# Optimization experiments

Measured on AMD Instinct MI355X. Metric: run time of the kernel, lower is better.

## Reference

```python
import jax, jax.numpy as jnp
import numpy as np

N_NODES = 12288
N_EDGES = 393216
LATENT = 128
EDGE_F = 4


def setup_inputs() -> dict:
    key = jax.random.key(0)
    k1, k2, k3, k4 = jax.random.split(key, 4)
    z = jax.random.normal(k1, (N_NODES, LATENT), dtype=jnp.float32)
    edge_index = jax.random.randint(k2, (2, N_EDGES), 0, N_NODES, dtype=jnp.int64)
    edge_attr = jax.random.normal(k3, (N_EDGES, EDGE_F), dtype=jnp.float32)
    W = jax.random.normal(k4, (1, 2 * LATENT), dtype=jnp.float32) * (1.0 / np.sqrt(2 * LATENT))
    b = jnp.zeros((1,), dtype=jnp.float32)
    return {"z": z, "edge_index": edge_index, "edge_attr": edge_attr, "W": W, "b": b}


def reference(z, edge_index, edge_attr, W, b):
    # z: [N, D], edge_index: [2, E], edge_attr: [E, F], W: [1, 2D], b: [1]
    num_nodes = z.shape[0]
    row, col = edge_index[0], edge_index[1]
    # gather node embeddings per edge and apply tiny linear: [E, 2D] @ [2D, 1]
    edge_features = jnp.concatenate([z[row], z[col]], axis=1)
    specified_edge_probs = (edge_features @ W.T + b)[:, 0]  # [E]
    # scatter edge probs into dense NxN (indexed assignment, like torch)
    full_edge_probs = jnp.zeros((num_nodes, num_nodes), dtype=z.dtype).at[row, col].set(specified_edge_probs)
    # to_dense_adj scatter-adds edge_attr -> [N, N, F]; sum(dim=3) commutes, so add summed attr
    adj = jnp.zeros((num_nodes, num_nodes), dtype=edge_attr.dtype).at[row, col].add(edge_attr.sum(axis=1))
    return adj + full_edge_probs
```

## Files before the change

### kernel.cpp

```cpp
#include <hip/hip_runtime.h>

#define N_NODES 12288
#define N_EDGES 393216
#define LATENT  128
#define BCAP    128
#define ROWS    4
#define RSLOTS  128
#define NCHUNK  (N_NODES / 4)
#define NBMW    (NCHUNK / 32)
#define DOT_BLOCKS (N_NODES / 4)
#define BKT_BLOCKS (N_EDGES / 256)


__global__ void dots_and_bucket(const float* __restrict__ z, const float* __restrict__ W,
                                const int* __restrict__ ei, const float* __restrict__ ea,
                                float* __restrict__ s1, float* __restrict__ s2,
                                unsigned int* __restrict__ cnt,
                                unsigned long long* __restrict__ bpack) {
    if (blockIdx.x < DOT_BLOCKS) {
        int node = (int)(blockIdx.x * 4 + (threadIdx.x >> 6));
        int lane = (int)(threadIdx.x & 63);
        const float* zr = z + (size_t)node * LATENT;
        float a  = zr[lane];
        float bb = zr[lane + 64];
        float p1 = a * W[lane]       + bb * W[lane + 64];
        float p2 = a * W[lane + 128] + bb * W[lane + 192];
        #pragma unroll
        for (int off = 32; off > 0; off >>= 1) {
            p1 += __shfl_down(p1, off, 64);
            p2 += __shfl_down(p2, off, 64);
        }
        if (lane == 0) { s1[node] = p1; s2[node] = p2; }
    } else {
        int e = (int)((blockIdx.x - DOT_BLOCKS) * 256 + threadIdx.x);
        unsigned int r = (unsigned int)ei[e];
        unsigned int c = (unsigned int)ei[e + N_EDGES];
        float4 a4 = ((const float4*)ea)[e];
        float s = a4.x + a4.y + a4.z + a4.w;
        unsigned int pos = atomicAdd(&cnt[r], 1u);
        bpack[(size_t)r * BCAP + pos] =
            ((unsigned long long)c << 32) | (unsigned long long)__float_as_uint(s);
    }
}

__global__ __launch_bounds__(256) void row_fill(const unsigned int* __restrict__ cnt,
                                                const unsigned long long* __restrict__ bpack,
                                                const float* __restrict__ s1,
                                                const float* __restrict__ s2,
                                                const float* __restrict__ bptr,
                                                float* __restrict__ out) {
    __shared__ unsigned int hcol[ROWS][RSLOTS];
    __shared__ float        hval[ROWS][RSLOTS];
    __shared__ unsigned int bm[ROWS][NBMW];
    int r0 = (int)blockIdx.x * ROWS;
    int t  = (int)threadIdx.x;

    for (int i = t; i < ROWS * RSLOTS; i += 256) {
        ((unsigned int*)hcol)[i] = 0u;
        ((float*)hval)[i] = 0.f;
    }
    for (int i = t; i < ROWS * NBMW; i += 256) ((unsigned int*)bm)[i] = 0u;
    __syncthreads();

    float bias = bptr[0];
    #pragma unroll
    for (int rr = 0; rr < ROWS; rr++) {
        int r = r0 + rr;
        unsigned int deg = cnt[r];
        float s1b = s1[r] + bias;
        const unsigned long long* seg = bpack + (size_t)r * BCAP;
        for (unsigned int i = (unsigned int)t; i < deg; i += 256u) {
            unsigned long long p = seg[i];
            unsigned int c = (unsigned int)(p >> 32);
            float v = __uint_as_float((unsigned int)p);
            unsigned int h = (c * 2654435761u) >> 25;
            for (;;) {
                unsigned int prev = atomicCAS(&hcol[rr][h], 0u, c + 1u);
                if (prev == 0u) {
                    v += s1b + s2[c];
                    atomicAdd(&hval[rr][h], v);
                    atomicOr(&bm[rr][c >> 7], 1u << ((c >> 2) & 31));
                    break;
                }
                if (prev == c + 1u) { atomicAdd(&hval[rr][h], v); break; }
                h = (h + 1u) & (RSLOTS - 1u);
            }
        }
    }
    __syncthreads();

    #pragma unroll
    for (int rr = 0; rr < ROWS; rr++) {
        float4* out4 = (float4*)(out + (size_t)(r0 + rr) * N_NODES);
        #pragma unroll
        for (int i = 0; i < 12; i++) {
            int j = t + i * 256;
            float4 v = make_float4(0.f, 0.f, 0.f, 0.f);
            if (bm[rr][j >> 5] & (1u << (j & 31))) {
                float* vp = (float*)&v;
                #pragma unroll
                for (int k = 0; k < 4; k++) {
                    unsigned int c = ((unsigned int)j << 2) + (unsigned int)k;
                    unsigned int h = (c * 2654435761u) >> 25;
                    for (;;) {
                        unsigned int pc = hcol[rr][h];
                        if (pc == 0u) break;
                        if (pc == c + 1u) { vp[k] = hval[rr][h]; break; }
                        h = (h + 1u) & (RSLOTS - 1u);
                    }
                }
            }
            out4[j] = v;
        }
    }
}

extern "C" void kernel_launch(void* const* d_in, const int* in_sizes, int n_in,
                              void* d_out, int out_size, void* d_ws, size_t ws_size,
                              hipStream_t stream) {
    const float* z  = (const float*)d_in[0];
    const int*   ei = (const int*)d_in[1];
    const float* ea = (const float*)d_in[2];
    const float* W  = (const float*)d_in[3];
    const float* b  = (const float*)d_in[4];
    float* out = (float*)d_out;

    char* ws = (char*)d_ws;
    float*              s1    = (float*)(ws + 0);
    float*              s2    = (float*)(ws + 49152);
    unsigned int*       cnt   = (unsigned int*)(ws + 98304);
    unsigned long long* bpack = (unsigned long long*)(ws + 147456);

    hipMemsetAsync(cnt, 0, N_NODES * sizeof(unsigned int), stream);
    dots_and_bucket<<<DOT_BLOCKS + BKT_BLOCKS, 256, 0, stream>>>(z, W, ei, ea, s1, s2, cnt, bpack);
    row_fill<<<N_NODES / ROWS, 256, 0, stream>>>(cnt, bpack, s1, s2, b, out);
}
```

Before: 647.9 us.

## Double-buffer row hash tables and precompute edge probs in bucketing

```diff
diff --git a/kernel.cpp b/kernel.cpp
--- a/kernel.cpp
+++ b/kernel.cpp
@@ -5,113 +5,142 @@
 #define LATENT  128
 #define BCAP    128
 #define ROWS    4
+#define G       6
 #define RSLOTS  128
-#define NCHUNK  (N_NODES / 4)
-#define NBMW    (NCHUNK / 32)
-#define DOT_BLOCKS (N_NODES / 4)
-#define BKT_BLOCKS (N_EDGES / 256)
+#define NBMW    96
+#define FILL_BLOCKS (N_NODES / (ROWS * G))
 
 
-__global__ void dots_and_bucket(const float* __restrict__ z, const float* __restrict__ W,
-                                const int* __restrict__ ei, const float* __restrict__ ea,
-                                float* __restrict__ s1, float* __restrict__ s2,
-                                unsigned int* __restrict__ cnt,
-                                unsigned long long* __restrict__ bpack) {
-    if (blockIdx.x < DOT_BLOCKS) {
-        int node = (int)(blockIdx.x * 4 + (threadIdx.x >> 6));
-        int lane = (int)(threadIdx.x & 63);
-        const float* zr = z + (size_t)node * LATENT;
-        float a  = zr[lane];
-        float bb = zr[lane + 64];
-        float p1 = a * W[lane]       + bb * W[lane + 64];
-        float p2 = a * W[lane + 128] + bb * W[lane + 192];
-        #pragma unroll
-        for (int off = 32; off > 0; off >>= 1) {
-            p1 += __shfl_down(p1, off, 64);
-            p2 += __shfl_down(p2, off, 64);
-        }
-        if (lane == 0) { s1[node] = p1; s2[node] = p2; }
-    } else {
-        int e = (int)((blockIdx.x - DOT_BLOCKS) * 256 + threadIdx.x);
-        unsigned int r = (unsigned int)ei[e];
-        unsigned int c = (unsigned int)ei[e + N_EDGES];
-        float4 a4 = ((const float4*)ea)[e];
-        float s = a4.x + a4.y + a4.z + a4.w;
-        unsigned int pos = atomicAdd(&cnt[r], 1u);
-        bpack[(size_t)r * BCAP + pos] =
-            ((unsigned long long)c << 32) | (unsigned long long)__float_as_uint(s);
+__global__ __launch_bounds__(256) void node_dots(const float* __restrict__ z,
+                                                 const float* __restrict__ W,
+                                                 float* __restrict__ s1, float* __restrict__ s2) {
+    int node = (int)(blockIdx.x * 4 + (threadIdx.x >> 6));
+    int lane = (int)(threadIdx.x & 63);
+    const float* zr = z + (size_t)node * LATENT;
+    float a  = zr[lane];
+    float bb = zr[lane + 64];
+    float p1 = a * W[lane]       + bb * W[lane + 64];
+    float p2 = a * W[lane + 128] + bb * W[lane + 192];
+    #pragma unroll
+    for (int off = 32; off > 0; off >>= 1) {
+        p1 += __shfl_down(p1, off, 64);
+        p2 += __shfl_down(p2, off, 64);
     }
+    if (lane == 0) { s1[node] = p1; s2[node] = p2; }
+}
+
+__global__ void bucket_edges(const int* __restrict__ ei, const float* __restrict__ ea,
+                             const float* __restrict__ s1, const float* __restrict__ s2,
+                             const float* __restrict__ bptr,
+                             unsigned int* __restrict__ cnt,
+                             unsigned long long* __restrict__ bpack,
+                             float* __restrict__ bprob) {
+    int e = (int)(blockIdx.x * blockDim.x + threadIdx.x);
+    unsigned int r = (unsigned int)ei[e];
+    unsigned int c = (unsigned int)ei[e + N_EDGES];
+    float4 a4 = ((const float4*)ea)[e];
+    float s = a4.x + a4.y + a4.z + a4.w;
+    float prob = s1[r] + s2[c] + bptr[0];
+    unsigned int pos = atomicAdd(&cnt[r], 1u);
+    bpack[(size_t)r * BCAP + pos] = ((unsigned long long)c << 32) | (unsigned long long)__float_as_uint(s);
+    bprob[(size_t)r * BCAP + pos] = prob;
 }
 
 __global__ __launch_bounds__(256) void row_fill(const unsigned int* __restrict__ cnt,
                                                 const unsigned long long* __restrict__ bpack,
-                                                const float* __restrict__ s1,
-                                                const float* __restrict__ s2,
-                                                const float* __restrict__ bptr,
+                                                const float* __restrict__ bprob,
                                                 float* __restrict__ out) {
-    __shared__ unsigned int hcol[ROWS][RSLOTS];
-    __shared__ float        hval[ROWS][RSLOTS];
-    __shared__ unsigned int bm[ROWS][NBMW];
-    int r0 = (int)blockIdx.x * ROWS;
-    int t  = (int)threadIdx.x;
+    __shared__ unsigned int hcol[2][ROWS][RSLOTS];
+    __shared__ float        hval[2][ROWS][RSLOTS];
+    __shared__ unsigned int bm[2][ROWS][NBMW];
+    int t    = (int)threadIdx.x;
+    int rw   = t >> 6;
+    int lane = t & 63;
+    int base = (int)blockIdx.x * (ROWS * G);
 
-    for (int i = t; i < ROWS * RSLOTS; i += 256) {
-        ((unsigned int*)hcol)[i] = 0u;
-        ((float*)hval)[i] = 0.f;
+    for (int i = t; i < 2 * ROWS * RSLOTS; i += 256) {
+        (&hcol[0][0][0])[i] = 0u;
+        (&hval[0][0][0])[i] = 0.f;
     }
-    for (int i = t; i < ROWS * NBMW; i += 256) ((unsigned int*)bm)[i] = 0u;
+    for (int i = t; i < 2 * ROWS * NBMW; i += 256) (&bm[0][0][0])[i] = 0u;
     __syncthreads();
 
-    float bias = bptr[0];
-    #pragma unroll
-    for (int rr = 0; rr < ROWS; rr++) {
-        int r = r0 + rr;
+    auto insert = [&](unsigned long long pk, float prob, int b) {
+        unsigned int c = (unsigned int)(pk >> 32);
+        float v = __uint_as_float((unsigned int)pk);
+        unsigned int h = (c * 2654435761u) >> 25;
+        for (;;) {
+            unsigned int prev = atomicCAS(&hcol[b][rw][h], 0u, c + 1u);
+            if (prev == 0u) {
+                atomicAdd(&hval[b][rw][h], v + prob);
+                atomicOr(&bm[b][rw][c >> 7], 1u << ((c >> 2) & 31));
+                break;
+            }
+            if (prev == c + 1u) { atomicAdd(&hval[b][rw][h], v); break; }
+            h = (h + 1u) & (RSLOTS - 1u);
+        }
+    };
+
+    {
+        size_t r = (size_t)(base + rw);
         unsigned int deg = cnt[r];
-        float s1b = s1[r] + bias;
-        const unsigned long long* seg = bpack + (size_t)r * BCAP;
-        for (unsigned int i = (unsigned int)t; i < deg; i += 256u) {
-            unsigned long long p = seg[i];
-            unsigned int c = (unsigned int)(p >> 32);
-            float v = __uint_as_float((unsigned int)p);
-            unsigned int h = (c * 2654435761u) >> 25;
-            for (;;) {
-                unsigned int prev = atomicCAS(&hcol[rr][h], 0u, c + 1u);
-                if (prev == 0u) {
-                    v += s1b + s2[c];
-                    atomicAdd(&hval[rr][h], v);
-                    atomicOr(&bm[rr][c >> 7], 1u << ((c >> 2) & 31));
-                    break;
-                }
-                if (prev == c + 1u) { atomicAdd(&hval[rr][h], v); break; }
-                h = (h + 1u) & (RSLOTS - 1u);
-            }
-        }
+        unsigned long long e0 = bpack[r * BCAP + lane];
+        unsigned long long e1 = bpack[r * BCAP + lane + 64];
+        float p0 = bprob[r * BCAP + lane];
+        float p1 = bprob[r * BCAP + lane + 64];
+        if ((unsigned int)lane < deg)       insert(e0, p0, 0);
+        if ((unsigned int)(lane + 64) < deg) insert(e1, p1, 0);
     }
     __syncthreads();
 
-    #pragma unroll
-    for (int rr = 0; rr < ROWS; rr++) {
-        float4* out4 = (float4*)(out + (size_t)(r0 + rr) * N_NODES);
+    for (int g = 0; g < G; ++g) {
+        int cur = g & 1;
+        unsigned int ndeg = 0;
+        unsigned long long f0 = 0, f1 = 0;
+        float q0 = 0.f, q1 = 0.f;
+        if (g + 1 < G) {
+            size_t r = (size_t)(base + (g + 1) * ROWS + rw);
+            ndeg = cnt[r];
+            f0 = bpack[r * BCAP + lane];
+            f1 = bpack[r * BCAP + lane + 64];
+            q0 = bprob[r * BCAP + lane];
+            q1 = bprob[r * BCAP + lane + 64];
+        }
         #pragma unroll
-        for (int i = 0; i < 12; i++) {
-            int j = t + i * 256;
-            float4 v = make_float4(0.f, 0.f, 0.f, 0.f);
-            if (bm[rr][j >> 5] & (1u << (j & 31))) {
-                float* vp = (float*)&v;
-                #pragma unroll
-                for (int k = 0; k < 4; k++) {
-                    unsigned int c = ((unsigned int)j << 2) + (unsigned int)k;
-                    unsigned int h = (c * 2654435761u) >> 25;
-                    for (;;) {
-                        unsigned int pc = hcol[rr][h];
-                        if (pc == 0u) break;
-                        if (pc == c + 1u) { vp[k] = hval[rr][h]; break; }
-                        h = (h + 1u) & (RSLOTS - 1u);
+        for (int rr = 0; rr < ROWS; ++rr) {
+            float4* out4 = (float4*)(out + (size_t)(base + g * ROWS + rr) * N_NODES);
+            #pragma unroll
+            for (int i = 0; i < 12; ++i) {
+                int j = t + i * 256;
+                float4 v = make_float4(0.f, 0.f, 0.f, 0.f);
+                if (bm[cur][rr][j >> 5] & (1u << (j & 31))) {
+                    float* vp = (float*)&v;
+                    #pragma unroll
+                    for (int k = 0; k < 4; ++k) {
+                        unsigned int c = ((unsigned int)j << 2) + (unsigned int)k;
+                        unsigned int h = (c * 2654435761u) >> 25;
+                        for (;;) {
+                            unsigned int pc = hcol[cur][rr][h];
+                            if (pc == 0u) break;
+                            if (pc == c + 1u) { vp[k] = hval[cur][rr][h]; break; }
+                            h = (h + 1u) & (RSLOTS - 1u);
+                        }
                     }
                 }
+                out4[j] = v;
             }
-            out4[j] = v;
         }
+        __syncthreads();
+        for (int i = t; i < ROWS * RSLOTS; i += 256) {
+            (&hcol[cur][0][0])[i] = 0u;
+            (&hval[cur][0][0])[i] = 0.f;
+        }
+        for (int i = t; i < ROWS * NBMW; i += 256) (&bm[cur][0][0])[i] = 0u;
+        if (g + 1 < G) {
+            if ((unsigned int)lane < ndeg)        insert(f0, q0, 1 - cur);
+            if ((unsigned int)(lane + 64) < ndeg) insert(f1, q1, 1 - cur);
+        }
+        __syncthreads();
     }
 }
 
@@ -130,8 +159,10 @@
     float*              s2    = (float*)(ws + 49152);
     unsigned int*       cnt   = (unsigned int*)(ws + 98304);
     unsigned long long* bpack = (unsigned long long*)(ws + 147456);
+    float*              bprob = (float*)(ws + 147456 + 12582912);
 
     hipMemsetAsync(cnt, 0, N_NODES * sizeof(unsigned int), stream);
-    dots_and_bucket<<<DOT_BLOCKS + BKT_BLOCKS, 256, 0, stream>>>(z, W, ei, ea, s1, s2, cnt, bpack);
-    row_fill<<<N_NODES / ROWS, 256, 0, stream>>>(cnt, bpack, s1, s2, b, out);
+    node_dots<<<N_NODES / 4, 256, 0, stream>>>(z, W, s1, s2);
+    bucket_edges<<<N_EDGES / 256, 256, 0, stream>>>(ei, ea, s1, s2, b, cnt, bpack, bprob);
+    row_fill<<<FILL_BLOCKS, 256, 0, stream>>>(cnt, bpack, bprob, out);
 }
```

Measured after the change: 661.1 us. +2.0%, slower.
